# Kernel tuning notes

Hardware: AMD Instinct MI355X
Metric: run time of the kernel (lower is better)

## Reference

```python
import jax, jax.numpy as jnp
from jax import lax
import numpy as np

# Model dims (see shape_source)
D_MODEL = 768
N_LAYERS = 8
D_STATE = 16
EXPAND = 2
D_INNER = EXPAND * D_MODEL          # 1536
DT_RANK = (D_MODEL + 15) // 16       # 48
D_CONV = 4
PATCH = 16
IMG = 224
CH = 3
BATCH = 8


def rmsnorm(x, w, eps=1e-5):
    return x * lax.rsqrt(jnp.mean(x * x, axis=-1, keepdims=True) + eps) * w


def patch_embed(img, w, b):
    # img: [B,C,H,W] -> tokens [B, N, d_model]
    x = lax.conv_general_dilated(img, w, (PATCH, PATCH), 'VALID',
                                 dimension_numbers=('NCHW', 'OIHW', 'NCHW'))
    x = x + b[None, :, None, None]
    Bsz = img.shape[0]
    return x.reshape(Bsz, D_MODEL, -1).transpose(0, 2, 1)


def mamba_block(x, in_w, cw, cb, xw, dtw, dtb, a_log, d_p, ow):
    # x: [B, L, d_model]
    Bsz, L, _ = x.shape
    xz = x @ in_w.T                                   # [B,L,2*ED]
    xin, z = jnp.split(xz, 2, axis=-1)
    # causal depthwise conv over L
    xc = lax.conv_general_dilated(xin.transpose(0, 2, 1), cw, (1,),
                                  [(D_CONV - 1, 0)],
                                  dimension_numbers=('NCH', 'OIH', 'NCH'),
                                  feature_group_count=D_INNER)
    xin = jax.nn.silu((xc + cb[None, :, None]).transpose(0, 2, 1))  # [B,L,ED]
    dbc = xin @ xw.T                                  # [B,L,dt_rank+2N]
    delta, Bm, Cm = jnp.split(dbc, [DT_RANK, DT_RANK + D_STATE], axis=-1)
    delta = jax.nn.softplus(delta @ dtw.T + dtb)      # [B,L,ED]
    A = -jnp.exp(a_log)                               # [ED,N]
    dA = jnp.exp(delta[..., None] * A)                # [B,L,ED,N]
    dBx = (delta * xin)[..., None] * Bm[:, :, None, :]  # [B,L,ED,N]

    def step(h, inp):
        a, bx = inp
        h = a * h + bx
        return h, h

    h0 = jnp.zeros((Bsz, D_INNER, D_STATE), x.dtype)
    _, hs = lax.scan(step, h0, (dA.transpose(1, 0, 2, 3), dBx.transpose(1, 0, 2, 3)))
    y = jnp.einsum('lben,bln->ble', hs, Cm)           # [B,L,ED]
    y = y + d_p * xin
    y = y * jax.nn.silu(z)
    return y @ ow.T                                   # [B,L,d_model]


def setup_inputs() -> dict:
    key = jax.random.key(0)
    ks = jax.random.split(key, 16)
    s = 0.02
    nl = N_LAYERS
    inp = {
        'rgb': jax.random.normal(ks[0], (BATCH, CH, IMG, IMG), jnp.float32),
        't': jax.random.normal(ks[1], (BATCH, CH, IMG, IMG), jnp.float32),
        'pe_w': jax.random.normal(ks[2], (D_MODEL, CH, PATCH, PATCH), jnp.float32) * s,
        'pe_b': jnp.zeros((D_MODEL,), jnp.float32),
        'in_proj_w': jax.random.normal(ks[3], (nl, 2 * D_INNER, D_MODEL), jnp.float32) * s,
        'conv_w': jax.random.normal(ks[4], (nl, D_INNER, 1, D_CONV), jnp.float32) * s,
        'conv_b': jnp.zeros((nl, D_INNER), jnp.float32),
        'x_proj_w': jax.random.normal(ks[5], (nl, DT_RANK + 2 * D_STATE, D_INNER), jnp.float32) * s,
        'dt_proj_w': jax.random.normal(ks[6], (nl, D_INNER, DT_RANK), jnp.float32) * s,
        'dt_proj_b': jax.random.normal(ks[7], (nl, D_INNER), jnp.float32) * s,
        'A_log': jnp.log(jnp.broadcast_to(jnp.arange(1.0, D_STATE + 1.0), (nl, D_INNER, D_STATE))),
        'D': jnp.ones((nl, D_INNER), jnp.float32),
        'out_proj_w': jax.random.normal(ks[8], (nl, D_MODEL, D_INNER), jnp.float32) * s,
        'norm_w': jnp.ones((nl, D_MODEL), jnp.float32),
    }
    return inp


def reference(rgb, t, pe_w, pe_b, in_proj_w, conv_w, conv_b, x_proj_w,
              dt_proj_w, dt_proj_b, A_log, D, out_proj_w, norm_w):
    rt = patch_embed(rgb, pe_w, pe_b)   # [B,196,768]
    tt = patch_embed(t, pe_w, pe_b)
    x = jnp.concatenate([rt, tt], axis=1)  # [B,392,768]
    for i in range(N_LAYERS):
        x = x + mamba_block(rmsnorm(x, norm_w[i]), in_proj_w[i], conv_w[i],
                            conv_b[i], x_proj_w[i], dt_proj_w[i], dt_proj_b[i],
                            A_log[i], D[i], out_proj_w[i])
    Bsz = rgb.shape[0]
    # [B,2N,D] -> [B,2N,D,1] -> transpose(0,3) -> [1,2N,D,B] -> [2B,C,H,W]
    out = jnp.transpose(x[..., None], (3, 1, 2, 0)).reshape(2 * Bsz, CH, IMG, IMG)
    return out[:Bsz], out[Bsz:]
```

## Files before the change

kernel.cpp:

```cpp
#include <hip/hip_runtime.h>
#include <cstddef>
#include <cstdint>

#define L_TOK 392
#define BATCH 8
#define DM    768
#define ED    1536
#define NST   16
#define DTR   48
#define ROWS  (BATCH * L_TOK)

#define C_CH 8
#define CLEN 49
#define EGB  24

#define XP_Z  8


typedef unsigned short ushortT;
typedef __bf16 bf16x8 __attribute__((ext_vector_type(8)));
typedef unsigned short us8 __attribute__((ext_vector_type(8)));
typedef unsigned short us4 __attribute__((ext_vector_type(4)));
typedef float f32x4 __attribute__((ext_vector_type(4)));

#define LOG2E 1.4426950408889634f

__device__ __forceinline__ float bf2f(ushortT u) {
    union { unsigned int i; float f; } v; v.i = ((unsigned int)u) << 16; return v.f;
}
__device__ __forceinline__ ushortT f2bf(float f) {
    union { float f; unsigned int i; } v; v.f = f;
    unsigned int r = v.i + 0x7FFFu + ((v.i >> 16) & 1u);
    return (ushortT)(r >> 16);
}

enum { EPI_STORE = 0, EPI_BIAS = 1, EPI_BIAS_SOFTPLUS = 2, EPI_ADD = 3 };

template <int EPI, bool C_BF, bool SPLIT, bool ATOMIC, bool PARTIAL>
__global__ __launch_bounds__(256)
void gemm_mfma(const ushortT* __restrict__ A, int lda,
               const float* __restrict__ W, int ldw,
               const float* __restrict__ bias,
               void* __restrict__ Cv, void* __restrict__ Cv2, int ldc,
               int M, int N, int K, int kchunk)
{
    __shared__ ushortT As[2][128 * 40];
    __shared__ ushortT Ws[2][128 * 40];

    const int tid  = threadIdx.x;
    const int lane = tid & 63;
    const int wave = tid >> 6;
    const int wm   = wave >> 1;
    const int wn   = wave & 1;
    const int quad = lane >> 4;
    const int l16  = lane & 15;

    const int m0 = blockIdx.y * 128;
    const int n0 = blockIdx.x * 128;
    const int kb = blockIdx.z * kchunk;
    const int KT = kchunk / 32;

    const int ar    = tid >> 1;
    const int ahalf = tid & 1;
    const int wr    = tid >> 3;
    const int wc    = (tid & 7) * 4;

    const int gm_a = m0 + ar;
    const ushortT* aptr = A + (size_t)gm_a * lda + ahalf * 16;

    us8 a0r = {0,0,0,0,0,0,0,0}, a1r = {0,0,0,0,0,0,0,0};
    float4 wfr[4];

    auto g_load = [&](int k0) {
        if (gm_a < M) {
            const ushortT* src = aptr + k0;
            a0r = *(const us8*)(src);
            a1r = *(const us8*)(src + 8);
        }
#pragma unroll
        for (int it = 0; it < 4; ++it) {
            int row = it * 32 + wr;
            wfr[it] = (n0 + row < N)
                ? *(const float4*)(W + (size_t)(n0 + row) * ldw + k0 + wc)
                : make_float4(0.f, 0.f, 0.f, 0.f);
        }
    };
    auto l_store = [&](int buf) {
        *(us8*)&As[buf][ar * 40 + ahalf * 16]     = a0r;
        *(us8*)&As[buf][ar * 40 + ahalf * 16 + 8] = a1r;
#pragma unroll
        for (int it = 0; it < 4; ++it) {
            int row = it * 32 + wr;
            float4 f = wfr[it];
            us4 h; h.x = f2bf(f.x); h.y = f2bf(f.y); h.z = f2bf(f.z); h.w = f2bf(f.w);
            *(us4*)&Ws[buf][row * 40 + wc] = h;
        }
    };

    f32x4 acc[4][4] = {};

    g_load(kb);
    l_store(0);
    __syncthreads();

    for (int kt = 0; kt < KT; ++kt) {
        const int cur = kt & 1;
        if (kt + 1 < KT) g_load(kb + (kt + 1) * 32);

        bf16x8 af[4], bw[4];
#pragma unroll
        for (int t = 0; t < 4; ++t) {
            us8 ta = *(const us8*)&As[cur][(wm * 64 + t * 16 + l16) * 40 + quad * 8];
            af[t] = __builtin_bit_cast(bf16x8, ta);
            us8 tb = *(const us8*)&Ws[cur][(wn * 64 + t * 16 + l16) * 40 + quad * 8];
            bw[t] = __builtin_bit_cast(bf16x8, tb);
        }
#pragma unroll
        for (int i = 0; i < 4; ++i)
#pragma unroll
            for (int j = 0; j < 4; ++j)
                acc[i][j] = __builtin_amdgcn_mfma_f32_16x16x32_bf16(
                    af[i], bw[j], acc[i][j], 0, 0, 0);

        if (kt + 1 < KT) l_store(cur ^ 1);
        __syncthreads();
    }

#pragma unroll
    for (int i = 0; i < 4; ++i) {
#pragma unroll
        for (int r = 0; r < 4; ++r) {
            int gm = m0 + wm * 64 + i * 16 + quad * 4 + r;
            if (gm >= M) continue;
#pragma unroll
            for (int j = 0; j < 4; ++j) {
                int gn = n0 + wn * 64 + j * 16 + l16;
                if (gn >= N) continue;
                float v = acc[i][j][r];
                if (EPI == EPI_BIAS) v += bias[gn];
                void* dst = Cv;
                int cn = gn;
                if (SPLIT && gn >= ED) { dst = Cv2; cn = gn - ED; }
                size_t off = (size_t)gm * ldc + cn;
                if (PARTIAL) {
                    ((float*)dst)[(size_t)blockIdx.z * M * ldc + off] = v;
                } else if (ATOMIC) {
                    atomicAdd((float*)dst + off, v);
                } else if (C_BF) {
                    ((ushortT*)dst)[off] = f2bf(v);
                } else {
                    float* p = (float*)dst + off;
                    *p = (EPI == EPI_ADD) ? v + *p : v;
                }
            }
        }
    }
}

__global__ __launch_bounds__(256)
void reduce_partials_kernel(const float* __restrict__ P, float* __restrict__ dbc)
{
    int idx = blockIdx.x * 256 + threadIdx.x;
    if (idx >= ROWS * 80) return;
    float s = 0.f;
#pragma unroll
    for (int z = 0; z < XP_Z; ++z)
        s += P[(size_t)z * ROWS * 80 + idx];
    dbc[idx] = s;
}

template <int EPI, bool A_BF, bool C_BF>
__global__ __launch_bounds__(256)
void gemm_nt(const void* __restrict__ Av, int lda,
             const float* __restrict__ W, int ldw,
             const float* __restrict__ bias,
             void* __restrict__ Cv, int ldc,
             int M, int N, int K)
{
    __shared__ float As[16][68];
    __shared__ float Bs[16][68];
    const int tid = threadIdx.x;
    const int tx  = tid & 15;
    const int ty  = tid >> 4;
    const int bm  = blockIdx.y * 64;
    const int bn  = blockIdx.x * 64;
    const int lr  = tid >> 2;
    const int lk  = (tid & 3) * 4;

    float acc[4][4] = {};

    for (int k0 = 0; k0 < K; k0 += 16) {
        float a0 = 0.f, a1 = 0.f, a2 = 0.f, a3 = 0.f;
        float w0 = 0.f, w1 = 0.f, w2 = 0.f, w3 = 0.f;
        int ga = bm + lr;
        if (ga < M) {
            if (A_BF) {
                const ushortT* A = (const ushortT*)Av;
                ushort4 t = *(const ushort4*)(A + (size_t)ga * lda + k0 + lk);
                a0 = bf2f(t.x); a1 = bf2f(t.y); a2 = bf2f(t.z); a3 = bf2f(t.w);
            } else {
                const float* A = (const float*)Av;
                float4 t = *(const float4*)(A + (size_t)ga * lda + k0 + lk);
                a0 = t.x; a1 = t.y; a2 = t.z; a3 = t.w;
            }
        }
        int gw = bn + lr;
        if (gw < N) {
            float4 t = *(const float4*)(W + (size_t)gw * ldw + k0 + lk);
            w0 = t.x; w1 = t.y; w2 = t.z; w3 = t.w;
        }
        As[lk + 0][lr] = a0; As[lk + 1][lr] = a1;
        As[lk + 2][lr] = a2; As[lk + 3][lr] = a3;
        Bs[lk + 0][lr] = w0; Bs[lk + 1][lr] = w1;
        Bs[lk + 2][lr] = w2; Bs[lk + 3][lr] = w3;
        __syncthreads();
#pragma unroll
        for (int k = 0; k < 16; ++k) {
            float4 a4 = *(const float4*)&As[k][ty * 4];
            float4 b4 = *(const float4*)&Bs[k][tx * 4];
            float a[4] = {a4.x, a4.y, a4.z, a4.w};
            float b[4] = {b4.x, b4.y, b4.z, b4.w};
#pragma unroll
            for (int i = 0; i < 4; ++i)
#pragma unroll
                for (int j = 0; j < 4; ++j)
                    acc[i][j] += a[i] * b[j];
        }
        __syncthreads();
    }

#pragma unroll
    for (int i = 0; i < 4; ++i) {
        int gm = bm + ty * 4 + i;
        if (gm >= M) continue;
#pragma unroll
        for (int j = 0; j < 4; ++j) {
            int gn = bn + tx * 4 + j;
            if (gn >= N) continue;
            float v = acc[i][j];
            if (EPI == EPI_BIAS) v += bias[gn];
            if (EPI == EPI_BIAS_SOFTPLUS) {
                v += bias[gn];
                v = fmaxf(v, 0.f) + log1pf(expf(-fabsf(v)));
            }
            size_t off = (size_t)gm * ldc + gn;
            if (C_BF) {
                ((ushortT*)Cv)[off] = f2bf(v);
            } else {
                float* p = (float*)Cv + off;
                *p = (EPI == EPI_ADD) ? v + *p : v;
            }
        }
    }
}

__global__ __launch_bounds__(256)
void rmsnorm_kernel(const float* __restrict__ x, const float* __restrict__ w,
                    ushortT* __restrict__ xn)
{
    int r = blockIdx.x;
    const float* xr = x + (size_t)r * DM;
    float v[3];
    float s = 0.f;
#pragma unroll
    for (int i = 0; i < 3; ++i) {
        v[i] = xr[threadIdx.x + i * 256];
        s += v[i] * v[i];
    }
#pragma unroll
    for (int o = 32; o > 0; o >>= 1) s += __shfl_down(s, o, 64);
    __shared__ float wsum[4];
    __shared__ float scale_s;
    int wave = threadIdx.x >> 6;
    if ((threadIdx.x & 63) == 0) wsum[wave] = s;
    __syncthreads();
    if (threadIdx.x == 0) {
        float t = wsum[0] + wsum[1] + wsum[2] + wsum[3];
        scale_s = rsqrtf(t * (1.f / 768.f) + 1e-5f);
    }
    __syncthreads();
    float sc = scale_s;
#pragma unroll
    for (int i = 0; i < 3; ++i) {
        int d = threadIdx.x + i * 256;
        xn[(size_t)r * DM + d] = f2bf(v[i] * sc * w[d]);
    }
}

__global__ __launch_bounds__(256)
void conv_silu_kernel(const ushortT* __restrict__ xc, const float* __restrict__ cw,
                      const float* __restrict__ cb, ushortT* __restrict__ xin)
{
    int idx = blockIdx.x * 256 + threadIdx.x;
    if (idx >= ROWS * ED) return;
    int e = idx % ED;
    int r = idx / ED;
    int l = r % L_TOK;
    float w0 = cw[e * 4 + 0], w1 = cw[e * 4 + 1];
    float w2 = cw[e * 4 + 2], w3 = cw[e * 4 + 3];
    const ushortT* base = xc + (size_t)r * ED + e;
    float acc = cb[e] + w3 * bf2f(base[0]);
    if (l >= 1) acc += w2 * bf2f(base[-(ptrdiff_t)ED]);
    if (l >= 2) acc += w1 * bf2f(base[-(ptrdiff_t)(2 * ED)]);
    if (l >= 3) acc += w0 * bf2f(base[-(ptrdiff_t)(3 * ED)]);
    xin[(size_t)r * ED + e] = f2bf(acc / (1.f + __expf(-acc)));
}

__global__ __launch_bounds__(64)
void scan_part1(const ushortT* __restrict__ delta, const ushortT* __restrict__ xin,
                const float* __restrict__ dbc, const float* __restrict__ a_log,
                float* __restrict__ hend, float* __restrict__ sdl)
{
    __shared__ float BsL[CLEN * 16];
    const int tid = threadIdx.x;
    const int bid = blockIdx.x;
    const int eg = bid % EGB;
    const int c  = (bid / EGB) % C_CH;
    const int b  = bid / (EGB * C_CH);
    const int e  = eg * 64 + tid;
    const int l0 = c * CLEN;
    const int rb = b * L_TOK + l0;

    for (int i = tid; i < CLEN * 16; i += 64) {
        int s = i >> 4, n = i & 15;
        BsL[i] = dbc[(size_t)(rb + s) * 80 + 48 + n];
    }
    __syncthreads();

    float a[16];
    const float* ar = a_log + (size_t)e * 16;
#pragma unroll
    for (int n = 0; n < 16; ++n) a[n] = -__expf(ar[n]) * LOG2E;

    float h[16];
#pragma unroll
    for (int n = 0; n < 16; ++n) h[n] = 0.f;
    float sum_dl = 0.f;

    const size_t base = (size_t)rb * ED + e;
    float rdl[7], rxi[7];
#pragma unroll
    for (int j = 0; j < 7; ++j) {
        rdl[j] = bf2f(delta[base + (size_t)j * ED]);
        rxi[j] = bf2f(xin[base + (size_t)j * ED]);
    }
    for (int s0 = 0; s0 < CLEN; s0 += 7) {
#pragma unroll
        for (int j = 0; j < 7; ++j) {
            const int s = s0 + j;
            float dl = rdl[j], xi = rxi[j];
            int sp = s + 7; if (sp > CLEN - 1) sp = CLEN - 1;
            rdl[j] = bf2f(delta[base + (size_t)sp * ED]);
            rxi[j] = bf2f(xin[base + (size_t)sp * ED]);
            float dlxi = dl * xi;
            sum_dl += dl;
#pragma unroll
            for (int n = 0; n < 16; ++n)
                h[n] = __builtin_amdgcn_exp2f(dl * a[n]) * h[n] + dlxi * BsL[s * 16 + n];
        }
    }

    float* hp = hend + (((size_t)b * ED + e) * C_CH + c) * 16;
#pragma unroll
    for (int n = 0; n < 16; ++n) hp[n] = h[n];
    sdl[((size_t)b * ED + e) * C_CH + c] = sum_dl;
}

__global__ __launch_bounds__(64)
void scan_part2(const ushortT* __restrict__ delta, const ushortT* __restrict__ xin,
                const float* __restrict__ dbc, const ushortT* __restrict__ zb,
                const float* __restrict__ a_log, const float* __restrict__ dvec,
                const float* __restrict__ hend, const float* __restrict__ sdl,
                ushortT* __restrict__ y)
{
    __shared__ float BsL[CLEN * 16];
    __shared__ float CsL[CLEN * 16];
    const int tid = threadIdx.x;
    const int bid = blockIdx.x;
    const int eg = bid % EGB;
    const int c  = (bid / EGB) % C_CH;
    const int b  = bid / (EGB * C_CH);
    const int e  = eg * 64 + tid;
    const int l0 = c * CLEN;
    const int rb = b * L_TOK + l0;

    for (int i = tid; i < CLEN * 16; i += 64) {
        int s = i >> 4, n = i & 15;
        size_t row = (size_t)(rb + s) * 80;
        BsL[i] = dbc[row + 48 + n];
        CsL[i] = dbc[row + 64 + n];
    }
    __syncthreads();

    float a[16];
    const float* ar = a_log + (size_t)e * 16;
#pragma unroll
    for (int n = 0; n < 16; ++n) a[n] = -__expf(ar[n]) * LOG2E;
    const float dcf = dvec[e];

    float h[16];
#pragma unroll
    for (int n = 0; n < 16; ++n) h[n] = 0.f;
    const float* hb = hend + (((size_t)b * ED + e) * C_CH) * 16;
    const float* sb = sdl + ((size_t)b * ED + e) * C_CH;
    for (int cc = 0; cc < c; ++cc) {
        float sv = sb[cc];
#pragma unroll
        for (int n = 0; n < 16; ++n)
            h[n] = __builtin_amdgcn_exp2f(a[n] * sv) * h[n] + hb[cc * 16 + n];
    }

    const size_t base = (size_t)rb * ED + e;
    float rdl[7], rxi[7], rz[7];
#pragma unroll
    for (int j = 0; j < 7; ++j) {
        rdl[j] = bf2f(delta[base + (size_t)j * ED]);
        rxi[j] = bf2f(xin[base + (size_t)j * ED]);
        rz[j]  = bf2f(zb[base + (size_t)j * ED]);
    }
    for (int s0 = 0; s0 < CLEN; s0 += 7) {
#pragma unroll
        for (int j = 0; j < 7; ++j) {
            const int s = s0 + j;
            float dl = rdl[j], xi = rxi[j], z = rz[j];
            int sp = s + 7; if (sp > CLEN - 1) sp = CLEN - 1;
            rdl[j] = bf2f(delta[base + (size_t)sp * ED]);
            rxi[j] = bf2f(xin[base + (size_t)sp * ED]);
            rz[j]  = bf2f(zb[base + (size_t)sp * ED]);
            float dlxi = dl * xi;
            float yv = 0.f;
#pragma unroll
            for (int n = 0; n < 16; ++n) {
                h[n] = __builtin_amdgcn_exp2f(dl * a[n]) * h[n] + dlxi * BsL[s * 16 + n];
                yv += h[n] * CsL[s * 16 + n];
            }
            yv += dcf * xi;
            float sz = z / (1.f + __expf(-z));
            y[base + (size_t)s * ED] = f2bf(yv * sz);
        }
    }
}

__global__ __launch_bounds__(256)
void im2col_kernel(const float* __restrict__ rgb, const float* __restrict__ timg,
                   ushortT* __restrict__ P)
{
    int idx = blockIdx.x * 256 + threadIdx.x;
    if (idx >= ROWS * DM) return;
    int k = idx % DM;
    int r = idx / DM;
    int b = r / L_TOK;
    int l = r % L_TOK;
    const float* img = (l < 196) ? rgb : timg;
    int p  = (l < 196) ? l : l - 196;
    int py = p / 14, px = p % 14;
    int c  = k >> 8;
    int ph = (k >> 4) & 15;
    int pw = k & 15;
    P[idx] = f2bf(img[(((size_t)b * 3 + c) * 224 + (py * 16 + ph)) * 224 + (px * 16 + pw)]);
}

__global__ __launch_bounds__(256)
void out_transpose_kernel(const float* __restrict__ x, float* __restrict__ out)
{
    int idx = blockIdx.x * 256 + threadIdx.x;
    if (idx >= ROWS * DM) return;
    int b = idx & 7;
    int d = (idx >> 3) % DM;
    int l = idx / (8 * DM);
    out[idx] = x[((size_t)(b * L_TOK + l)) * DM + d];
}

extern "C" void kernel_launch(void* const* d_in, const int* in_sizes, int n_in,
                              void* d_out, int out_size, void* d_ws, size_t ws_size,
                              hipStream_t stream)
{
    (void)in_sizes; (void)n_in; (void)out_size; (void)ws_size;

    const float* rgb  = (const float*)d_in[0];
    const float* timg = (const float*)d_in[1];
    const float* pe_w = (const float*)d_in[2];
    const float* pe_b = (const float*)d_in[3];
    const float* in_w = (const float*)d_in[4];
    const float* cw   = (const float*)d_in[5];
    const float* cb   = (const float*)d_in[6];
    const float* xw   = (const float*)d_in[7];
    const float* dtw  = (const float*)d_in[8];
    const float* dtb  = (const float*)d_in[9];
    const float* alog = (const float*)d_in[10];
    const float* dvec = (const float*)d_in[11];
    const float* ow   = (const float*)d_in[12];
    const float* nw   = (const float*)d_in[13];

    char* p = (char*)d_ws;
    float*   X   = (float*)p;    p += (size_t)ROWS * DM * 4;
    ushortT* XC  = (ushortT*)p;  p += (size_t)ROWS * ED * 2;
    ushortT* Zb  = (ushortT*)p;  p += (size_t)ROWS * ED * 2;
    ushortT* XIN = (ushortT*)p;  p += (size_t)ROWS * ED * 2;
    ushortT* DEL = (ushortT*)p;  p += (size_t)ROWS * ED * 2;
    float*   DBC = (float*)p;    p += (size_t)ROWS * 80 * 4;
    ushortT* XN  = DEL;

    float* POUT = (float*)d_out;
    float* HEND = (float*)d_out;
    float* SDL  = HEND + (size_t)BATCH * ED * C_CH * 16;

    dim3 b256(256);
    const int MT = (ROWS + 127) / 128;
    const int SCAN_BLOCKS = BATCH * C_CH * EGB;

    im2col_kernel<<<(ROWS * DM + 255) / 256, b256, 0, stream>>>(rgb, timg, XC);
    gemm_mfma<EPI_BIAS, false, false, false, false><<<dim3(DM / 128, MT), b256, 0, stream>>>(
        XC, DM, pe_w, DM, pe_b, X, nullptr, DM, ROWS, DM, DM, DM);

    for (int i = 0; i < 8; ++i) {
        const float* in_wi = in_w + (size_t)i * 2 * ED * DM;
        const float* cwi   = cw   + (size_t)i * ED * 4;
        const float* cbi   = cb   + (size_t)i * ED;
        const float* xwi   = xw   + (size_t)i * 80 * ED;
        const float* dtwi  = dtw  + (size_t)i * ED * DTR;
        const float* dtbi  = dtb  + (size_t)i * ED;
        const float* ali   = alog + (size_t)i * ED * NST;
        const float* dvi   = dvec + (size_t)i * ED;
        const float* owi   = ow   + (size_t)i * DM * ED;
        const float* nwi   = nw   + (size_t)i * DM;

        rmsnorm_kernel<<<ROWS, b256, 0, stream>>>(X, nwi, XN);
        gemm_mfma<EPI_STORE, true, true, false, false><<<dim3(2 * ED / 128, MT), b256, 0, stream>>>(
            XN, DM, in_wi, DM, nullptr, XC, Zb, ED, ROWS, 2 * ED, DM, DM);
        conv_silu_kernel<<<(ROWS * ED + 255) / 256, b256, 0, stream>>>(
            XC, cwi, cbi, XIN);
        gemm_mfma<EPI_STORE, false, false, false, true><<<dim3(1, MT, XP_Z), b256, 0, stream>>>(
            XIN, ED, xwi, ED, nullptr, POUT, nullptr, 80, ROWS, 80, ED, ED / XP_Z);
        reduce_partials_kernel<<<(ROWS * 80 + 255) / 256, b256, 0, stream>>>(
            POUT, DBC);
        gemm_nt<EPI_BIAS_SOFTPLUS, false, true><<<dim3(ED / 64, ROWS / 64), b256, 0, stream>>>(
            DBC, 80, dtwi, DTR, dtbi, DEL, ED, ROWS, ED, DTR);
        scan_part1<<<SCAN_BLOCKS, 64, 0, stream>>>(
            DEL, XIN, DBC, ali, HEND, SDL);
        scan_part2<<<SCAN_BLOCKS, 64, 0, stream>>>(
            DEL, XIN, DBC, Zb, ali, dvi, HEND, SDL, XC);
        gemm_mfma<EPI_ADD, false, false, true, false><<<dim3(DM / 128, MT, 2), b256, 0, stream>>>(
            XC, ED, owi, ED, nullptr, X, nullptr, DM, ROWS, DM, ED, ED / 2);
    }

    out_transpose_kernel<<<(ROWS * DM + 255) / 256, b256, 0, stream>>>(
        X, (float*)d_out);
}
```

Before: 1.849 ms.

## Pre-convert GEMM weights to bf16, swizzle blocks across XCDs, deepen load pipeline

A new kernel converts the fp32 weights to bf16 once per layer, writing them into scratch buffers. The GEMM then loads bf16 weights directly, which halves weight traffic and removes the per-tile fp32-to-bf16 conversion from the main loop. The GEMM also remaps workgroups across the 8 XCDs for L2 locality and prefetches two k-tiles ahead with ping-pong registers, and the x_proj split-K factor drops from 8 to 6. The cost is an extra conversion launch per layer. Workspace aliasing reuses XIN, DBC, Zb and the output buffer, so correctness depends on those buffers not being live while the converted weights are in use.

New measurement: 1.956 ms. +5.8%, slower.

```diff
diff --git a/kernel.cpp b/kernel.cpp
--- a/kernel.cpp
+++ b/kernel.cpp
@@ -14,7 +14,7 @@
 #define CLEN 49
 #define EGB  24
 
-#define XP_Z  8
+#define XP_Z  6
 
 
 typedef unsigned short ushortT;
@@ -36,10 +36,26 @@
 
 enum { EPI_STORE = 0, EPI_BIAS = 1, EPI_BIAS_SOFTPLUS = 2, EPI_ADD = 3 };
 
+__global__ __launch_bounds__(256)
+void convert3_kernel(const float* __restrict__ s0, ushortT* __restrict__ d0, int n0,
+                     const float* __restrict__ s1, ushortT* __restrict__ d1, int n1,
+                     const float* __restrict__ s2, ushortT* __restrict__ d2, int n2)
+{
+    int idx = blockIdx.x * 256 + threadIdx.x;
+    const float* s; ushortT* d;
+    if (idx < n0) { s = s0; d = d0; }
+    else if (idx < n0 + n1) { idx -= n0; s = s1; d = d1; }
+    else if (idx < n0 + n1 + n2) { idx -= n0 + n1; s = s2; d = d2; }
+    else return;
+    float4 f = *(const float4*)(s + (size_t)idx * 4);
+    us4 h; h.x = f2bf(f.x); h.y = f2bf(f.y); h.z = f2bf(f.z); h.w = f2bf(f.w);
+    *(us4*)(d + (size_t)idx * 4) = h;
+}
+
 template <int EPI, bool C_BF, bool SPLIT, bool ATOMIC, bool PARTIAL>
 __global__ __launch_bounds__(256)
 void gemm_mfma(const ushortT* __restrict__ A, int lda,
-               const float* __restrict__ W, int ldw,
+               const ushortT* __restrict__ W, int ldw,
                const float* __restrict__ bias,
                void* __restrict__ Cv, void* __restrict__ Cv2, int ldc,
                int M, int N, int K, int kchunk)
@@ -55,64 +71,62 @@
     const int quad = lane >> 4;
     const int l16  = lane & 15;
 
-    const int m0 = blockIdx.y * 128;
-    const int n0 = blockIdx.x * 128;
+    const int gx   = gridDim.x;
+    const int nwg  = gx * gridDim.y;
+    const int flat = blockIdx.y * gx + blockIdx.x;
+    const int q = nwg >> 3, r = nwg & 7;
+    const int xcd = flat & 7, sidx = flat >> 3;
+    const int swz = (xcd < r ? xcd * (q + 1) : r * (q + 1) + (xcd - r) * q) + sidx;
+
+    const int m0 = (swz / gx) * 128;
+    const int n0 = (swz % gx) * 128;
     const int kb = blockIdx.z * kchunk;
     const int KT = kchunk / 32;
 
     const int ar    = tid >> 1;
     const int ahalf = tid & 1;
-    const int wr    = tid >> 3;
-    const int wc    = (tid & 7) * 4;
 
     const int gm_a = m0 + ar;
+    const bool a_ok = gm_a < M;
     const ushortT* aptr = A + (size_t)gm_a * lda + ahalf * 16;
-
-    us8 a0r = {0,0,0,0,0,0,0,0}, a1r = {0,0,0,0,0,0,0,0};
-    float4 wfr[4];
-
-    auto g_load = [&](int k0) {
-        if (gm_a < M) {
+    const int gw_w = n0 + ar;
+    const bool w_ok = gw_w < N;
+    const ushortT* wptr = W + (size_t)gw_w * ldw + ahalf * 16;
+
+    us8 a0A = {0,0,0,0,0,0,0,0}, a1A = {0,0,0,0,0,0,0,0};
+    us8 w0A = {0,0,0,0,0,0,0,0}, w1A = {0,0,0,0,0,0,0,0};
+    us8 a0B = {0,0,0,0,0,0,0,0}, a1B = {0,0,0,0,0,0,0,0};
+    us8 w0B = {0,0,0,0,0,0,0,0}, w1B = {0,0,0,0,0,0,0,0};
+
+    auto g_load = [&](int k0, us8& A0, us8& A1, us8& W0, us8& W1) {
+        if (a_ok) {
             const ushortT* src = aptr + k0;
-            a0r = *(const us8*)(src);
-            a1r = *(const us8*)(src + 8);
-        }
-#pragma unroll
-        for (int it = 0; it < 4; ++it) {
-            int row = it * 32 + wr;
-            wfr[it] = (n0 + row < N)
-                ? *(const float4*)(W + (size_t)(n0 + row) * ldw + k0 + wc)
-                : make_float4(0.f, 0.f, 0.f, 0.f);
+            A0 = *(const us8*)(src);
+            A1 = *(const us8*)(src + 8);
+        }
+        if (w_ok) {
+            const ushortT* src = wptr + k0;
+            W0 = *(const us8*)(src);
+            W1 = *(const us8*)(src + 8);
         }
     };
-    auto l_store = [&](int buf) {
-        *(us8*)&As[buf][ar * 40 + ahalf * 16]     = a0r;
-        *(us8*)&As[buf][ar * 40 + ahalf * 16 + 8] = a1r;
-#pragma unroll
-        for (int it = 0; it < 4; ++it) {
-            int row = it * 32 + wr;
-            float4 f = wfr[it];
-            us4 h; h.x = f2bf(f.x); h.y = f2bf(f.y); h.z = f2bf(f.z); h.w = f2bf(f.w);
-            *(us4*)&Ws[buf][row * 40 + wc] = h;
-        }
+    auto l_store = [&](int buf, const us8& A0, const us8& A1,
+                       const us8& W0, const us8& W1) {
+        *(us8*)&As[buf][ar * 40 + ahalf * 16]     = A0;
+        *(us8*)&As[buf][ar * 40 + ahalf * 16 + 8] = A1;
+        *(us8*)&Ws[buf][ar * 40 + ahalf * 16]     = W0;
+        *(us8*)&Ws[buf][ar * 40 + ahalf * 16 + 8] = W1;
     };
 
     f32x4 acc[4][4] = {};
 
-    g_load(kb);
-    l_store(0);
-    __syncthreads();
-
-    for (int kt = 0; kt < KT; ++kt) {
-        const int cur = kt & 1;
-        if (kt + 1 < KT) g_load(kb + (kt + 1) * 32);
-
+    auto compute = [&](int buf) {
         bf16x8 af[4], bw[4];
 #pragma unroll
         for (int t = 0; t < 4; ++t) {
-            us8 ta = *(const us8*)&As[cur][(wm * 64 + t * 16 + l16) * 40 + quad * 8];
+            us8 ta = *(const us8*)&As[buf][(wm * 64 + t * 16 + l16) * 40 + quad * 8];
             af[t] = __builtin_bit_cast(bf16x8, ta);
-            us8 tb = *(const us8*)&Ws[cur][(wn * 64 + t * 16 + l16) * 40 + quad * 8];
+            us8 tb = *(const us8*)&Ws[buf][(wn * 64 + t * 16 + l16) * 40 + quad * 8];
             bw[t] = __builtin_bit_cast(bf16x8, tb);
         }
 #pragma unroll
@@ -121,22 +135,36 @@
             for (int j = 0; j < 4; ++j)
                 acc[i][j] = __builtin_amdgcn_mfma_f32_16x16x32_bf16(
                     af[i], bw[j], acc[i][j], 0, 0, 0);
-
-        if (kt + 1 < KT) l_store(cur ^ 1);
+    };
+
+    g_load(kb, a0A, a1A, w0A, w1A);
+    l_store(0, a0A, a1A, w0A, w1A);
+    if (KT > 1) g_load(kb + 32, a0B, a1B, w0B, w1B);
+    __syncthreads();
+
+    for (int kt = 0; kt < KT; kt += 2) {
+        if (kt + 2 < KT) g_load(kb + (kt + 2) * 32, a0A, a1A, w0A, w1A);
+        compute(0);
+        if (kt + 1 < KT) l_store(1, a0B, a1B, w0B, w1B);
         __syncthreads();
+        if (kt + 1 >= KT) break;
+        if (kt + 3 < KT) g_load(kb + (kt + 3) * 32, a0B, a1B, w0B, w1B);
+        compute(1);
+        if (kt + 2 < KT) l_store(0, a0A, a1A, w0A, w1A);
+        __syncthreads();
     }
 
 #pragma unroll
     for (int i = 0; i < 4; ++i) {
 #pragma unroll
-        for (int r = 0; r < 4; ++r) {
-            int gm = m0 + wm * 64 + i * 16 + quad * 4 + r;
+        for (int r2 = 0; r2 < 4; ++r2) {
+            int gm = m0 + wm * 64 + i * 16 + quad * 4 + r2;
             if (gm >= M) continue;
 #pragma unroll
             for (int j = 0; j < 4; ++j) {
                 int gn = n0 + wn * 64 + j * 16 + l16;
                 if (gn >= N) continue;
-                float v = acc[i][j][r];
+                float v = acc[i][j][r2];
                 if (EPI == EPI_BIAS) v += bias[gn];
                 void* dst = Cv;
                 int cn = gn;
@@ -501,17 +529,31 @@
     float*   DBC = (float*)p;    p += (size_t)ROWS * 80 * 4;
     ushortT* XN  = DEL;
 
+    ushortT* INWB = XIN;
+    ushortT* XWB  = (ushortT*)DBC;
+    ushortT* PEB  = Zb;
+
     float* POUT = (float*)d_out;
     float* HEND = (float*)d_out;
     float* SDL  = HEND + (size_t)BATCH * ED * C_CH * 16;
+    ushortT* OWB = (ushortT*)((char*)d_out +
+                   ((size_t)BATCH * ED * C_CH * 16 + (size_t)BATCH * ED * C_CH) * 4);
 
     dim3 b256(256);
     const int MT = (ROWS + 127) / 128;
     const int SCAN_BLOCKS = BATCH * C_CH * EGB;
 
+    const int PE_F4  = DM * DM / 4;
+    const int INW_F4 = 2 * ED * DM / 4;
+    const int XW_F4  = 80 * ED / 4;
+    const int OW_F4  = DM * ED / 4;
+    const int CVT_BLOCKS = (INW_F4 + XW_F4 + OW_F4 + 255) / 256;
+
+    convert3_kernel<<<(PE_F4 + 255) / 256, b256, 0, stream>>>(
+        pe_w, PEB, PE_F4, nullptr, nullptr, 0, nullptr, nullptr, 0);
     im2col_kernel<<<(ROWS * DM + 255) / 256, b256, 0, stream>>>(rgb, timg, XC);
     gemm_mfma<EPI_BIAS, false, false, false, false><<<dim3(DM / 128, MT), b256, 0, stream>>>(
-        XC, DM, pe_w, DM, pe_b, X, nullptr, DM, ROWS, DM, DM, DM);
+        XC, DM, PEB, DM, pe_b, X, nullptr, DM, ROWS, DM, DM, DM);
 
     for (int i = 0; i < 8; ++i) {
         const float* in_wi = in_w + (size_t)i * 2 * ED * DM;
@@ -525,13 +567,15 @@
         const float* owi   = ow   + (size_t)i * DM * ED;
         const float* nwi   = nw   + (size_t)i * DM;
 
+        convert3_kernel<<<CVT_BLOCKS, b256, 0, stream>>>(
+            in_wi, INWB, INW_F4, xwi, XWB, XW_F4, owi, OWB, OW_F4);
         rmsnorm_kernel<<<ROWS, b256, 0, stream>>>(X, nwi, XN);
         gemm_mfma<EPI_STORE, true, true, false, false><<<dim3(2 * ED / 128, MT), b256, 0, stream>>>(
-            XN, DM, in_wi, DM, nullptr, XC, Zb, ED, ROWS, 2 * ED, DM, DM);
+            XN, DM, INWB, DM, nullptr, XC, Zb, ED, ROWS, 2 * ED, DM, DM);
         conv_silu_kernel<<<(ROWS * ED + 255) / 256, b256, 0, stream>>>(
             XC, cwi, cbi, XIN);
         gemm_mfma<EPI_STORE, false, false, false, true><<<dim3(1, MT, XP_Z), b256, 0, stream>>>(
-            XIN, ED, xwi, ED, nullptr, POUT, nullptr, 80, ROWS, 80, ED, ED / XP_Z);
+            XIN, ED, XWB, ED, nullptr, POUT, nullptr, 80, ROWS, 80, ED, ED / XP_Z);
         reduce_partials_kernel<<<(ROWS * 80 + 255) / 256, b256, 0, stream>>>(
             POUT, DBC);
         gemm_nt<EPI_BIAS_SOFTPLUS, false, true><<<dim3(ED / 64, ROWS / 64), b256, 0, stream>>>(
@@ -541,7 +585,7 @@
         scan_part2<<<SCAN_BLOCKS, 64, 0, stream>>>(
             DEL, XIN, DBC, Zb, ali, dvi, HEND, SDL, XC);
         gemm_mfma<EPI_ADD, false, false, true, false><<<dim3(DM / 128, MT, 2), b256, 0, stream>>>(
-            XC, ED, owi, ED, nullptr, X, nullptr, DM, ROWS, DM, ED, ED / 2);
+            XC, ED, OWB, ED, nullptr, X, nullptr, DM, ROWS, DM, ED, ED / 2);
     }
 
     out_transpose_kernel<<<(ROWS * DM + 255) / 256, b256, 0, stream>>>(
```
